# Kernel tuning notes

Hardware: AMD Instinct MI355X
Metric: run time of the kernel (lower is better)

The kernel has to match this reference:

```python
import jax, jax.numpy as jnp
import numpy as np

BATCH = 1024


def setup_inputs() -> dict:
    key = jax.random.key(0)
    ks = jax.random.split(key, 8)
    piece_positions = jax.random.randint(ks[0], (BATCH, 64, 10), 0, 2) > 0  # bool occupancy
    king_positions = jax.random.randint(ks[1], (BATCH, 2), 0, 64, dtype=jnp.int32)
    input_weights = jax.random.randint(ks[2], (64, 641, 256), -32768, 32767, dtype=jnp.int16)
    input_bias = jnp.zeros((256,), dtype=jnp.int16)
    w1 = jax.random.randint(ks[3], (32, 512), -128, 127, dtype=jnp.int8)
    b1 = jnp.zeros((32,), dtype=jnp.int32)
    w2 = jax.random.randint(ks[4], (32, 32), -128, 127, dtype=jnp.int8)
    b2 = jnp.zeros((32,), dtype=jnp.int32)
    out_w = jax.random.randint(ks[5], (32,), -128, 127, dtype=jnp.int8)
    out_b = jnp.zeros((1,), dtype=jnp.int32)
    return {
        'piece_positions': piece_positions, 'king_positions': king_positions,
        'input_weights': input_weights, 'input_bias': input_bias,
        'w1': w1, 'b1': b1, 'w2': w2, 'b2': b2, 'out_w': out_w, 'out_b': out_b,
    }


def _fc(x, w, b):
    # int8 inputs/weights, int32 accumulate, floor-div 64, clamp to [0,127] -> int8
    y = x.astype(jnp.int32) @ w.T.astype(jnp.int32) + b
    y = jnp.floor_divide(y, 64)
    return jnp.clip(y, 0, 127).astype(jnp.int8)


def reference(piece_positions, king_positions, input_weights, input_bias,
              w1, b1, w2, b2, out_w, out_b):
    B = piece_positions.shape[0]
    pp = piece_positions.reshape(B, 640).astype(jnp.int32)  # flattened 64x10 HalfKP features

    def half(king_idx):
        wk = input_weights[king_idx]            # (B, 641, 256) gathered per-sample king table
        feats = wk[:, :640, :].astype(jnp.int32)
        kbias = wk[:, 640, :].astype(jnp.int32)
        return jnp.einsum('bf,bfd->bd', pp, feats) + kbias  # (B, 256)

    white = half(king_positions[:, 0])
    black = half(king_positions[:, 1])
    # int16 wraparound semantics of the original: accumulate in int32, mod-cast to int16
    acc = (white + black + input_bias.astype(jnp.int32)).astype(jnp.int16)

    x = jnp.clip(acc, 0, 127).astype(jnp.int8)
    x = jnp.concatenate([x, x], axis=1)  # (B, 512) side_to_move || other_side
    x = _fc(x, w1, b1)
    x = _fc(x, w2, b2)
    s = jnp.sum(x.astype(jnp.int32) * out_w.astype(jnp.int32)) + out_b  # scalar sum over batch too (as in source)
    return jnp.floor_divide(s, 16)  # shape (1,)
```

## Files before the change

kernel.cpp:

```cpp
#include <hip/hip_runtime.h>
#include <stdint.h>

#define NDIM  256
#define NFEAT 640
#define NROWS 641
#define SG    8
#define MAXG  16
#define MAXRPB 320

typedef unsigned short ushort4v __attribute__((ext_vector_type(4)));
typedef unsigned short ushort8v __attribute__((ext_vector_type(8)));

__global__ void nnue_bucket(const int* __restrict__ kp, const int* __restrict__ W32,
                            const int* __restrict__ pp32, int nslots,
                            int* __restrict__ ws,
                            int* __restrict__ king_start, int* __restrict__ slot_list,
                            int* __restrict__ slot_pos)
{
    __shared__ int cnt[64];
    __shared__ int off[64];
    const int t = threadIdx.x;
    if (t < 64) cnt[t] = 0;
    if (t == 0) {
        int raww = 0, rawpp = 0;
        for (int i = 0; i < 16; ++i) {
            const int v = W32[i];
            if (v > 32767 || v < -32768) raww = 1;
            const int u = pp32[i];
            if (u != 0 && u != 1) rawpp = 1;
        }
        ws[0] = 0; ws[1] = raww; ws[2] = rawpp;
    }
    __syncthreads();
    for (int s = t; s < nslots; s += 256) atomicAdd(&cnt[kp[s]], 1);
    __syncthreads();
    if (t == 0) {
        int run = 0;
        for (int k = 0; k < 64; ++k) { off[k] = run; king_start[k] = run; run += cnt[k]; }
        king_start[64] = run;
    }
    __syncthreads();
    for (int s = t; s < nslots; s += 256) {
        const int k = kp[s];
        const int pos = atomicAdd(&off[k], 1);
        slot_list[pos] = s;
        slot_pos[s] = pos;
    }
}

struct GatherLds {
    int samp[SG];
    unsigned mask[MAXRPB];
    unsigned red[4][SG][NDIM / 2];
};

template<bool RAWW, bool RAWPP>
__device__ __forceinline__ void gather_body(
    const void* __restrict__ ppv, const void* __restrict__ Wv,
    const int* __restrict__ king_start, const int* __restrict__ slot_list,
    unsigned short* __restrict__ partial, int nslots, int rp, GatherLds& sh)
{
    const int bid = blockIdx.x;
    const int k = bid & 63;
    const int rest = bid >> 6;
    const int p = rest & (rp - 1);
    const int gi = rest / rp;
    const int t = threadIdx.x, l = t & 63, g = t >> 6;

    const int s0 = king_start[k], s1 = king_start[k + 1];
    const int base = s0 + gi * SG;
    if (base >= s1) return;
    const int ns = min(SG, s1 - base);
    const unsigned emask = (ns >= 32) ? 0xFFFFFFFFu : ((1u << ns) - 1u);
    const int rpb = NFEAT / rp;
    const int r0 = p * rpb;

    if (t < SG) sh.samp[t] = slot_list[base + min(t, ns - 1)] >> 1;
    __syncthreads();

    for (int r = t; r < rpb; r += 256) {
        unsigned mm = 0;
        #pragma unroll
        for (int i = 0; i < SG; ++i) {
            const int s = sh.samp[i];
            int v;
            if (RAWPP) v = ((const uint8_t*)ppv)[(size_t)s * NFEAT + r0 + r];
            else       v = ((const int*)ppv)[(size_t)s * NFEAT + r0 + r];
            mm |= (v != 0 ? 1u : 0u) << i;
        }
        sh.mask[r] = mm & emask;
    }
    __syncthreads();

    ushort4v acc[SG];
    #pragma unroll
    for (int i = 0; i < SG; ++i) acc[i] = (ushort4v)0;

    const char* Wk = (const char*)Wv + (size_t)k * NROWS * NDIM * (RAWW ? 2 : 4);
    const int rows_per_wave = rpb / 4;
    const int lbeg = g * rows_per_wave;

    #pragma unroll 2
    for (int rr = 0; rr < rows_per_wave; ++rr) {
        const int lr = lbeg + rr;
        unsigned mm = sh.mask[lr];
        mm = __builtin_amdgcn_readfirstlane(mm);
        ushort4v w;
        if (RAWW) {
            w = *(const ushort4v*)(Wk + (size_t)(r0 + lr) * 512 + (size_t)l * 8);
        } else {
            const int4 u = *(const int4*)(Wk + (size_t)(r0 + lr) * 1024 + (size_t)l * 16);
            w.x = (unsigned short)u.x; w.y = (unsigned short)u.y;
            w.z = (unsigned short)u.z; w.w = (unsigned short)u.w;
        }
        #pragma unroll
        for (int i = 0; i < SG; ++i)
            if (mm & (1u << i)) acc[i] += w;
    }

    #pragma unroll
    for (int i = 0; i < SG; ++i)
        *(ushort4v*)&sh.red[g][i][2 * l] = acc[i];
    __syncthreads();

    const int i = t >> 5;
    const int j4 = (t & 31) * 4;
    if (i < ns) {
        ushort8v s = *(const ushort8v*)&sh.red[0][i][j4];
        #pragma unroll
        for (int g2 = 1; g2 < 4; ++g2) s += *(const ushort8v*)&sh.red[g2][i][j4];
        *(ushort8v*)&partial[((size_t)p * nslots + base + i) * NDIM + (size_t)(t & 31) * 8] = s;
    }
}

__global__ __launch_bounds__(256, 6) void nnue_gather(
    const void* __restrict__ pp, const void* __restrict__ W,
    const int* __restrict__ ws, const int* __restrict__ king_start,
    const int* __restrict__ slot_list, unsigned short* __restrict__ partial,
    int nslots, int rp)
{
    __shared__ GatherLds sh;
    const int raww = ws[1], rawpp = ws[2];
    if (raww) {
        if (rawpp) gather_body<true,  true >(pp, W, king_start, slot_list, partial, nslots, rp, sh);
        else       gather_body<true,  false>(pp, W, king_start, slot_list, partial, nslots, rp, sh);
    } else {
        if (rawpp) gather_body<false, true >(pp, W, king_start, slot_list, partial, nslots, rp, sh);
        else       gather_body<false, false>(pp, W, king_start, slot_list, partial, nslots, rp, sh);
    }
}

struct CombineLds {
    alignas(16) int8_t x[NDIM];
    int fc[256];
    alignas(4) int8_t x2[32];
};

template<bool RAWW>
__device__ __forceinline__ void combine_body(
    const unsigned short* __restrict__ partial, const int* __restrict__ slot_pos,
    const int* __restrict__ kp, const void* __restrict__ Wv,
    const void* __restrict__ ibv,
    const void* __restrict__ w1v, const int* __restrict__ b1,
    const void* __restrict__ w2v, const int* __restrict__ b2,
    const void* __restrict__ owv, int* __restrict__ ws, int nslots, int rp,
    CombineLds& sh)
{
    const int b = blockIdx.x;
    const int t = threadIdx.x;

    const int pos0 = slot_pos[2 * b + 0];
    const int pos1 = slot_pos[2 * b + 1];
    const int k0 = kp[2 * b + 0];
    const int k1 = kp[2 * b + 1];
    {
        unsigned tot = 0;
        for (int pi = 0; pi < rp; ++pi) {
            tot += partial[((size_t)pi * nslots + pos0) * NDIM + t];
            tot += partial[((size_t)pi * nslots + pos1) * NDIM + t];
        }
        if (RAWW) {
            const uint16_t* Wq = (const uint16_t*)Wv;
            tot += Wq[((size_t)k0 * NROWS + NFEAT) * NDIM + t];
            tot += Wq[((size_t)k1 * NROWS + NFEAT) * NDIM + t];
            tot += ((const uint16_t*)ibv)[t];
        } else {
            const int* Wq = (const int*)Wv;
            tot += (unsigned)Wq[((size_t)k0 * NROWS + NFEAT) * NDIM + t];
            tot += (unsigned)Wq[((size_t)k1 * NROWS + NFEAT) * NDIM + t];
            tot += (unsigned)((const int*)ibv)[t];
        }
        int v = (int)(int16_t)(uint16_t)tot;
        v = v < 0 ? 0 : (v > 127 ? 127 : v);
        sh.x[t] = (int8_t)v;
    }
    __syncthreads();

    {
        const int o = t >> 3, part = t & 7;
        int y = 0;
        const uint32_t* xw = (const uint32_t*)sh.x;
        if (RAWW) {
            const uint32_t* w1r = (const uint32_t*)((const char*)w1v + o * 512);
            #pragma unroll
            for (int i = 0; i < 8; ++i) {
                const int wi = part * 8 + i;
                const uint32_t xv = xw[wi];
                const uint32_t wa = w1r[wi];
                const uint32_t wb = w1r[64 + wi];
                #pragma unroll
                for (int jj = 0; jj < 4; ++jj) {
                    const int xj  = (int)((xv >> (8 * jj)) & 0xFFu);
                    const int waj = (int)(int8_t)(uint8_t)(wa >> (8 * jj));
                    const int wbj = (int)(int8_t)(uint8_t)(wb >> (8 * jj));
                    y += xj * (waj + wbj);
                }
            }
        } else {
            const int* w1r = (const int*)w1v + o * 512;
            #pragma unroll
            for (int i = 0; i < 8; ++i) {
                const int wi = part * 8 + i;
                const uint32_t xv = xw[wi];
                #pragma unroll
                for (int jj = 0; jj < 4; ++jj) {
                    const int xj = (int)((xv >> (8 * jj)) & 0xFFu);
                    y += xj * (w1r[wi * 4 + jj] + w1r[256 + wi * 8 / 2 + jj]);
                }
            }
        }
        sh.fc[t] = y;
    }
    __syncthreads();

    if (t < 32) {
        int y = b1[t];
        #pragma unroll
        for (int pq = 0; pq < 8; ++pq) y += sh.fc[t * 8 + pq];
        y >>= 6;
        y = y < 0 ? 0 : (y > 127 ? 127 : y);
        sh.x2[t] = (int8_t)y;
    }
    __syncthreads();

    if (t < 32) {
        int y = b2[t];
        const uint32_t* x2w = (const uint32_t*)sh.x2;
        if (RAWW) {
            const uint32_t* w2r = (const uint32_t*)((const char*)w2v + t * 32);
            #pragma unroll
            for (int i = 0; i < 8; ++i) {
                const uint32_t xv = x2w[i];
                const uint32_t wv = w2r[i];
                #pragma unroll
                for (int jj = 0; jj < 4; ++jj)
                    y += (int)((xv >> (8 * jj)) & 0xFFu) * (int)(int8_t)(uint8_t)(wv >> (8 * jj));
            }
        } else {
            const int* w2r = (const int*)w2v + t * 32;
            #pragma unroll
            for (int i = 0; i < 8; ++i) {
                const uint32_t xv = x2w[i];
                #pragma unroll
                for (int jj = 0; jj < 4; ++jj)
                    y += (int)((xv >> (8 * jj)) & 0xFFu) * w2r[i * 4 + jj];
            }
        }
        y >>= 6;
        y = y < 0 ? 0 : (y > 127 ? 127 : y);
        const int owx = RAWW ? (int)((const int8_t*)owv)[t] : ((const int*)owv)[t];
        int pr = y * owx;
        #pragma unroll
        for (int off = 16; off > 0; off >>= 1) pr += __shfl_down(pr, off, 32);
        if (t == 0) atomicAdd(ws, pr);
    }
}

__global__ __launch_bounds__(256) void nnue_combine(
    const unsigned short* __restrict__ partial, const int* __restrict__ slot_pos,
    const int* __restrict__ kp, const void* __restrict__ W,
    const void* __restrict__ ib,
    const void* __restrict__ w1, const int* __restrict__ b1,
    const void* __restrict__ w2, const int* __restrict__ b2,
    const void* __restrict__ ow, int* __restrict__ ws, int nslots, int rp)
{
    __shared__ CombineLds sh;
    if (ws[1]) combine_body<true >(partial, slot_pos, kp, W, ib, w1, b1, w2, b2, ow, ws, nslots, rp, sh);
    else       combine_body<false>(partial, slot_pos, kp, W, ib, w1, b1, w2, b2, ow, ws, nslots, rp, sh);
}

__global__ void nnue_finalize(const int* __restrict__ ws, const int* __restrict__ ob,
                              int* __restrict__ out) {
    out[0] = (ws[0] + ob[0]) >> 4;
}

struct SharedBuf {
    uint8_t pp[NFEAT];
    int     acc[4][NDIM];
    alignas(16) int8_t x[NDIM];
    int     fc[256];
    alignas(4) int8_t x2[32];
    int     list[4][160];
};

__global__ void detect_layout(const int* __restrict__ W32, const int* __restrict__ pp32,
                              int* __restrict__ ws) {
    int raww = 0, rawpp = 0;
    for (int i = 0; i < 16; ++i) {
        const int v = W32[i];
        if (v > 32767 || v < -32768) raww = 1;
        const int u = pp32[i];
        if (u != 0 && u != 1) rawpp = 1;
    }
    ws[0] = 0; ws[1] = raww; ws[2] = rawpp;
}

template<bool RAWW, bool RAWPP>
__device__ __forceinline__ void mono_body(
    const void* __restrict__ ppv, const int* __restrict__ kp,
    const void* __restrict__ Wv,  const void* __restrict__ ibv,
    const void* __restrict__ w1v, const int* __restrict__ b1,
    const void* __restrict__ w2v, const int* __restrict__ b2,
    const void* __restrict__ owv, int* __restrict__ ws, SharedBuf& sh)
{
    const int b = blockIdx.x;
    const int t = threadIdx.x;
    const int l = t & 63;
    const int g = t >> 6;

    if (RAWPP) {
        const uint32_t* src = (const uint32_t*)((const uint8_t*)ppv + (size_t)b * NFEAT);
        if (t < NFEAT / 4) ((uint32_t*)sh.pp)[t] = src[t];
    } else {
        const int* src = (const int*)ppv + (size_t)b * NFEAT;
        for (int i = t; i < NFEAT; i += 256) sh.pp[i] = (uint8_t)(src[i] != 0);
    }
    __syncthreads();

    const int base = g * 160;
    int cnt = 0;
    for (int c = 0; c < 160; c += 64) {
        const int idx = c + l;
        const bool flag = (idx < 160) && (sh.pp[base + idx] != 0);
        const unsigned long long mmask = __ballot(flag);
        const int pos = cnt + (int)__popcll(mmask & ((1ull << l) - 1ull));
        if (flag) sh.list[g][pos] = base + idx;
        cnt += (int)__popcll(mmask);
    }

    const int k0 = kp[b * 2 + 0];
    const int k1 = kp[b * 2 + 1];
    int a0 = 0, a1 = 0, a2 = 0, a3 = 0, a4 = 0, a5 = 0, a6 = 0, a7 = 0;

    if (RAWW) {
        const char* W0 = (const char*)Wv + (size_t)k0 * (NROWS * NDIM * 2);
        const char* W1 = (const char*)Wv + (size_t)k1 * (NROWS * NDIM * 2);
        const int lo = l * 8;
        auto step = [&](int f) {
            const uint2 u0 = *(const uint2*)(W0 + f * 512 + lo);
            const uint2 u1 = *(const uint2*)(W1 + f * 512 + lo);
            a0 += (int)(u0.x & 0xFFFFu); a1 += (int)(u0.x >> 16);
            a2 += (int)(u0.y & 0xFFFFu); a3 += (int)(u0.y >> 16);
            a4 += (int)(u1.x & 0xFFFFu); a5 += (int)(u1.x >> 16);
            a6 += (int)(u1.y & 0xFFFFu); a7 += (int)(u1.y >> 16);
        };
        int j = 0;
        for (; j + 4 <= cnt; j += 4) {
            const int f0 = sh.list[g][j], f1 = sh.list[g][j + 1];
            const int f2 = sh.list[g][j + 2], f3 = sh.list[g][j + 3];
            step(f0); step(f1); step(f2); step(f3);
        }
        for (; j < cnt; ++j) step(sh.list[g][j]);
    } else {
        const char* W0 = (const char*)Wv + (size_t)k0 * (NROWS * NDIM * 4);
        const char* W1 = (const char*)Wv + (size_t)k1 * (NROWS * NDIM * 4);
        const int lo = l * 16;
        auto step = [&](int f) {
            const int4 u0 = *(const int4*)(W0 + f * 1024 + lo);
            const int4 u1 = *(const int4*)(W1 + f * 1024 + lo);
            a0 += u0.x; a1 += u0.y; a2 += u0.z; a3 += u0.w;
            a4 += u1.x; a5 += u1.y; a6 += u1.z; a7 += u1.w;
        };
        int j = 0;
        for (; j + 4 <= cnt; j += 4) {
            const int f0 = sh.list[g][j], f1 = sh.list[g][j + 1];
            const int f2 = sh.list[g][j + 2], f3 = sh.list[g][j + 3];
            step(f0); step(f1); step(f2); step(f3);
        }
        for (; j < cnt; ++j) step(sh.list[g][j]);
    }

    sh.acc[g][4 * l + 0] = a0 + a4;
    sh.acc[g][4 * l + 1] = a1 + a5;
    sh.acc[g][4 * l + 2] = a2 + a6;
    sh.acc[g][4 * l + 3] = a3 + a7;
    __syncthreads();

    {
        const int d = t;
        int tot = sh.acc[0][d] + sh.acc[1][d] + sh.acc[2][d] + sh.acc[3][d];
        int kb0, kb1, ibx;
        if (RAWW) {
            const int16_t* Wq = (const int16_t*)Wv;
            kb0 = Wq[((size_t)k0 * NROWS + NFEAT) * NDIM + d];
            kb1 = Wq[((size_t)k1 * NROWS + NFEAT) * NDIM + d];
            ibx = ((const int16_t*)ibv)[d];
        } else {
            const int* Wq = (const int*)Wv;
            kb0 = Wq[((size_t)k0 * NROWS + NFEAT) * NDIM + d];
            kb1 = Wq[((size_t)k1 * NROWS + NFEAT) * NDIM + d];
            ibx = ((const int*)ibv)[d];
        }
        tot += kb0 + kb1 + ibx;
        int v = (int)(int16_t)(uint16_t)(uint32_t)tot;
        v = v < 0 ? 0 : (v > 127 ? 127 : v);
        sh.x[d] = (int8_t)v;
    }
    __syncthreads();

    {
        const int o = t >> 3, part = t & 7;
        int y = 0;
        const uint32_t* xw = (const uint32_t*)sh.x;
        if (RAWW) {
            const uint32_t* w1r = (const uint32_t*)((const char*)w1v + o * 512);
            #pragma unroll
            for (int i = 0; i < 8; ++i) {
                const int wi = part * 8 + i;
                const uint32_t xv = xw[wi];
                const uint32_t wa = w1r[wi];
                const uint32_t wb = w1r[64 + wi];
                #pragma unroll
                for (int jj = 0; jj < 4; ++jj) {
                    const int xj  = (int)((xv >> (8 * jj)) & 0xFFu);
                    const int waj = (int)(int8_t)(uint8_t)(wa >> (8 * jj));
                    const int wbj = (int)(int8_t)(uint8_t)(wb >> (8 * jj));
                    y += xj * (waj + wbj);
                }
            }
        } else {
            const int* w1r = (const int*)w1v + o * 512;
            #pragma unroll
            for (int i = 0; i < 8; ++i) {
                const int wi = part * 8 + i;
                const uint32_t xv = xw[wi];
                #pragma unroll
                for (int jj = 0; jj < 4; ++jj) {
                    const int xj = (int)((xv >> (8 * jj)) & 0xFFu);
                    y += xj * (w1r[wi * 4 + jj] + w1r[256 + wi * 4 + jj]);
                }
            }
        }
        sh.fc[t] = y;
    }
    __syncthreads();

    if (t < 32) {
        int y = b1[t];
        #pragma unroll
        for (int pq = 0; pq < 8; ++pq) y += sh.fc[t * 8 + pq];
        y >>= 6;
        y = y < 0 ? 0 : (y > 127 ? 127 : y);
        sh.x2[t] = (int8_t)y;
    }
    __syncthreads();

    if (t < 32) {
        int y = b2[t];
        const uint32_t* x2w = (const uint32_t*)sh.x2;
        if (RAWW) {
            const uint32_t* w2r = (const uint32_t*)((const char*)w2v + t * 32);
            #pragma unroll
            for (int i = 0; i < 8; ++i) {
                const uint32_t xv = x2w[i];
                const uint32_t wv = w2r[i];
                #pragma unroll
                for (int jj = 0; jj < 4; ++jj)
                    y += (int)((xv >> (8 * jj)) & 0xFFu) * (int)(int8_t)(uint8_t)(wv >> (8 * jj));
            }
        } else {
            const int* w2r = (const int*)w2v + t * 32;
            #pragma unroll
            for (int i = 0; i < 8; ++i) {
                const uint32_t xv = x2w[i];
                #pragma unroll
                for (int jj = 0; jj < 4; ++jj)
                    y += (int)((xv >> (8 * jj)) & 0xFFu) * w2r[i * 4 + jj];
            }
        }
        y >>= 6;
        y = y < 0 ? 0 : (y > 127 ? 127 : y);
        const int owx = RAWW ? (int)((const int8_t*)owv)[t] : ((const int*)owv)[t];
        int pr = y * owx;
        #pragma unroll
        for (int off = 16; off > 0; off >>= 1) pr += __shfl_down(pr, off, 32);
        if (t == 0) atomicAdd(ws, pr);
    }
}

__global__ __launch_bounds__(256, 4) void nnue_mono(
    const void* __restrict__ pp, const int* __restrict__ kp,
    const void* __restrict__ W,  const void* __restrict__ ib,
    const void* __restrict__ w1, const int* __restrict__ b1,
    const void* __restrict__ w2, const int* __restrict__ b2,
    const void* __restrict__ ow, int* __restrict__ ws)
{
    __shared__ SharedBuf sh;
    const int raww = ws[1], rawpp = ws[2];
    if (raww) {
        if (rawpp) mono_body<true,  true >(pp, kp, W, ib, w1, b1, w2, b2, ow, ws, sh);
        else       mono_body<true,  false>(pp, kp, W, ib, w1, b1, w2, b2, ow, ws, sh);
    } else {
        if (rawpp) mono_body<false, true >(pp, kp, W, ib, w1, b1, w2, b2, ow, ws, sh);
        else       mono_body<false, false>(pp, kp, W, ib, w1, b1, w2, b2, ow, ws, sh);
    }
}

extern "C" void kernel_launch(void* const* d_in, const int* in_sizes, int n_in,
                              void* d_out, int out_size, void* d_ws, size_t ws_size,
                              hipStream_t stream)
{
    const void* pp = d_in[0];
    const int*  kp = (const int*)d_in[1];
    const void* W  = d_in[2];
    const void* ib = d_in[3];
    const void* w1 = d_in[4];
    const int*  b1 = (const int*)d_in[5];
    const void* w2 = d_in[6];
    const int*  b2 = (const int*)d_in[7];
    const void* ow = d_in[8];
    const int*  ob = (const int*)d_in[9];
    int* ws  = (int*)d_ws;
    int* out = (int*)d_out;

    const int B = in_sizes[1] / 2;
    const int nslots = 2 * B;

    const size_t off_ks = 16;
    const size_t off_sl = 96;
    const size_t off_sp = off_sl + (size_t)nslots;
    const size_t off_pb = ((off_sp + (size_t)nslots + 255) / 256) * 256;
    const size_t need4 = (off_pb + (size_t)4 * nslots * (NDIM / 2)) * 4;
    const size_t need2 = (off_pb + (size_t)2 * nslots * (NDIM / 2)) * 4;

    int rp = 0;
    if (ws_size >= need4) rp = 4;
    else if (ws_size >= need2) rp = 2;

    if (rp) {
        int* king_start = ws + off_ks;
        int* slot_list  = ws + off_sl;
        int* slot_pos   = ws + off_sp;
        unsigned short* partial = (unsigned short*)(ws + off_pb);

        hipLaunchKernelGGL(nnue_bucket, dim3(1), dim3(256), 0, stream,
                           kp, (const int*)W, (const int*)pp, nslots,
                           ws, king_start, slot_list, slot_pos);
        hipLaunchKernelGGL(nnue_gather, dim3(64 * MAXG * rp), dim3(256), 0, stream,
                           pp, W, ws, king_start, slot_list, partial, nslots, rp);
        hipLaunchKernelGGL(nnue_combine, dim3(B), dim3(256), 0, stream,
                           partial, slot_pos, kp, W, ib, w1, b1, w2, b2, ow, ws, nslots, rp);
        hipLaunchKernelGGL(nnue_finalize, dim3(1), dim3(1), 0, stream, ws, ob, out);
    } else {
        hipLaunchKernelGGL(detect_layout, dim3(1), dim3(1), 0, stream,
                           (const int*)W, (const int*)pp, ws);
        hipLaunchKernelGGL(nnue_mono, dim3(B), dim3(256), 0, stream,
                           pp, kp, W, ib, w1, b1, w2, b2, ow, ws);
        hipLaunchKernelGGL(nnue_finalize, dim3(1), dim3(1), 0, stream, ws, ob, out);
    }
}
```

Measured before the change: 148.3 us.

## Fuse bucketing into gather, batch combine samples, and finalize via last-block ticket

Removes the single-block bucket kernel: each gather block now builds its own king's slot list in LDS with a wave ballot scan over all king indices, and loops over sample groups with a fixed stride instead of launching a sparse MAXG grid. Combine handles several samples per block, indexes partials by slot id directly, and writes the final output through a last-block atomic ticket, dropping the finalize kernel. The intent is fewer launches, fewer serialized single-block phases and fewer global atomics. In exchange every gather block redundantly scans all king positions, occupancy drops under the new launch bounds, and the fast path now requires at most 2048 slots.

```diff
diff --git a/kernel.cpp b/kernel.cpp
--- a/kernel.cpp
+++ b/kernel.cpp
@@ -5,148 +5,151 @@
 #define NFEAT 640
 #define NROWS 641
 #define SG    8
-#define MAXG  16
+#define GSTRIDE 4
 #define MAXRPB 320
+#define CPB   4
+#define MAXSLOTS 2048
 
 typedef unsigned short ushort4v __attribute__((ext_vector_type(4)));
 typedef unsigned short ushort8v __attribute__((ext_vector_type(8)));
 
-__global__ void nnue_bucket(const int* __restrict__ kp, const int* __restrict__ W32,
-                            const int* __restrict__ pp32, int nslots,
-                            int* __restrict__ ws,
-                            int* __restrict__ king_start, int* __restrict__ slot_list,
-                            int* __restrict__ slot_pos)
-{
-    __shared__ int cnt[64];
-    __shared__ int off[64];
-    const int t = threadIdx.x;
-    if (t < 64) cnt[t] = 0;
+struct GatherLds {
+    int flags[2];
+    int cnt;
+    unsigned short list[MAXSLOTS];
+    int samp[SG];
+    int slotid[SG];
+    unsigned mask[MAXRPB];
+    unsigned red[4][SG][NDIM / 2];
+};
+
+template<bool RAWW, bool RAWPP>
+__device__ __forceinline__ void gather_body(
+    const void* __restrict__ ppv, const void* __restrict__ Wv,
+    unsigned short* __restrict__ partial, int nslots, int rp, GatherLds& sh)
+{
+    const int bid = blockIdx.x;
+    const int k = bid & 63;
+    const int rest = bid >> 6;
+    const int p = rest & (rp - 1);
+    const int g0 = rest >> (rp == 4 ? 2 : 1);
+    const int t = threadIdx.x, l = t & 63, g = t >> 6;
+
+    const int cnt = sh.cnt;
+    const int rpb = NFEAT / rp;
+    const int r0 = p * rpb;
+    const int rows_per_wave = rpb / 4;
+    const int lbeg = g * rows_per_wave;
+    const char* Wk = (const char*)Wv + (size_t)k * NROWS * NDIM * (RAWW ? 2 : 4);
+
+    for (int gi = g0; gi * SG < cnt; gi += GSTRIDE) {
+        const int base = gi * SG;
+        const int ns = min(SG, cnt - base);
+        const unsigned emask = (1u << ns) - 1u;
+
+        if (t < SG) {
+            const int s = sh.list[base + min(t, ns - 1)];
+            sh.slotid[t] = s;
+            sh.samp[t] = s >> 1;
+        }
+        __syncthreads();
+
+        for (int r = t; r < rpb; r += 256) {
+            unsigned mm = 0;
+            #pragma unroll
+            for (int i = 0; i < SG; ++i) {
+                const int s = sh.samp[i];
+                int v;
+                if (RAWPP) v = ((const uint8_t*)ppv)[(size_t)s * NFEAT + r0 + r];
+                else       v = ((const int*)ppv)[(size_t)s * NFEAT + r0 + r];
+                mm |= (v != 0 ? 1u : 0u) << i;
+            }
+            sh.mask[r] = mm & emask;
+        }
+        __syncthreads();
+
+        ushort4v acc[SG];
+        #pragma unroll
+        for (int i = 0; i < SG; ++i) acc[i] = (ushort4v)0;
+
+        #pragma unroll 2
+        for (int rr = 0; rr < rows_per_wave; ++rr) {
+            const int lr = lbeg + rr;
+            unsigned mm = sh.mask[lr];
+            mm = __builtin_amdgcn_readfirstlane(mm);
+            ushort4v w;
+            if (RAWW) {
+                w = *(const ushort4v*)(Wk + (size_t)(r0 + lr) * 512 + (size_t)l * 8);
+            } else {
+                const int4 u = *(const int4*)(Wk + (size_t)(r0 + lr) * 1024 + (size_t)l * 16);
+                w.x = (unsigned short)u.x; w.y = (unsigned short)u.y;
+                w.z = (unsigned short)u.z; w.w = (unsigned short)u.w;
+            }
+            #pragma unroll
+            for (int i = 0; i < SG; ++i)
+                if (mm & (1u << i)) acc[i] += w;
+        }
+
+        #pragma unroll
+        for (int i = 0; i < SG; ++i)
+            *(ushort4v*)&sh.red[g][i][2 * l] = acc[i];
+        __syncthreads();
+
+        const int i = t >> 5;
+        const int j4 = (t & 31) * 4;
+        if (i < ns) {
+            ushort8v sv = *(const ushort8v*)&sh.red[0][i][j4];
+            #pragma unroll
+            for (int g2 = 1; g2 < 4; ++g2) sv += *(const ushort8v*)&sh.red[g2][i][j4];
+            *(ushort8v*)&partial[((size_t)p * nslots + sh.slotid[i]) * NDIM + (size_t)(t & 31) * 8] = sv;
+        }
+        __syncthreads();
+    }
+}
+
+__global__ __launch_bounds__(256, 4) void nnue_gather(
+    const void* __restrict__ pp, const int* __restrict__ kp,
+    const void* __restrict__ W, unsigned short* __restrict__ partial,
+    int* __restrict__ ws, int nslots, int rp)
+{
+    __shared__ GatherLds sh;
+    const int t = threadIdx.x, l = t & 63, g = t >> 6;
+    const int k = blockIdx.x & 63;
+
+    if (blockIdx.x == 0 && t == 0) { ws[0] = 0; ws[3] = 0; }
+
     if (t == 0) {
         int raww = 0, rawpp = 0;
+        const int* W32 = (const int*)W;
+        const int* pp32 = (const int*)pp;
         for (int i = 0; i < 16; ++i) {
             const int v = W32[i];
             if (v > 32767 || v < -32768) raww = 1;
             const int u = pp32[i];
             if (u != 0 && u != 1) rawpp = 1;
         }
-        ws[0] = 0; ws[1] = raww; ws[2] = rawpp;
-    }
-    __syncthreads();
-    for (int s = t; s < nslots; s += 256) atomicAdd(&cnt[kp[s]], 1);
-    __syncthreads();
-    if (t == 0) {
-        int run = 0;
-        for (int k = 0; k < 64; ++k) { off[k] = run; king_start[k] = run; run += cnt[k]; }
-        king_start[64] = run;
-    }
-    __syncthreads();
-    for (int s = t; s < nslots; s += 256) {
-        const int k = kp[s];
-        const int pos = atomicAdd(&off[k], 1);
-        slot_list[pos] = s;
-        slot_pos[s] = pos;
-    }
-}
-
-struct GatherLds {
-    int samp[SG];
-    unsigned mask[MAXRPB];
-    unsigned red[4][SG][NDIM / 2];
-};
-
-template<bool RAWW, bool RAWPP>
-__device__ __forceinline__ void gather_body(
-    const void* __restrict__ ppv, const void* __restrict__ Wv,
-    const int* __restrict__ king_start, const int* __restrict__ slot_list,
-    unsigned short* __restrict__ partial, int nslots, int rp, GatherLds& sh)
-{
-    const int bid = blockIdx.x;
-    const int k = bid & 63;
-    const int rest = bid >> 6;
-    const int p = rest & (rp - 1);
-    const int gi = rest / rp;
-    const int t = threadIdx.x, l = t & 63, g = t >> 6;
-
-    const int s0 = king_start[k], s1 = king_start[k + 1];
-    const int base = s0 + gi * SG;
-    if (base >= s1) return;
-    const int ns = min(SG, s1 - base);
-    const unsigned emask = (ns >= 32) ? 0xFFFFFFFFu : ((1u << ns) - 1u);
-    const int rpb = NFEAT / rp;
-    const int r0 = p * rpb;
-
-    if (t < SG) sh.samp[t] = slot_list[base + min(t, ns - 1)] >> 1;
-    __syncthreads();
-
-    for (int r = t; r < rpb; r += 256) {
-        unsigned mm = 0;
-        #pragma unroll
-        for (int i = 0; i < SG; ++i) {
-            const int s = sh.samp[i];
-            int v;
-            if (RAWPP) v = ((const uint8_t*)ppv)[(size_t)s * NFEAT + r0 + r];
-            else       v = ((const int*)ppv)[(size_t)s * NFEAT + r0 + r];
-            mm |= (v != 0 ? 1u : 0u) << i;
-        }
-        sh.mask[r] = mm & emask;
-    }
-    __syncthreads();
-
-    ushort4v acc[SG];
-    #pragma unroll
-    for (int i = 0; i < SG; ++i) acc[i] = (ushort4v)0;
-
-    const char* Wk = (const char*)Wv + (size_t)k * NROWS * NDIM * (RAWW ? 2 : 4);
-    const int rows_per_wave = rpb / 4;
-    const int lbeg = g * rows_per_wave;
-
-    #pragma unroll 2
-    for (int rr = 0; rr < rows_per_wave; ++rr) {
-        const int lr = lbeg + rr;
-        unsigned mm = sh.mask[lr];
-        mm = __builtin_amdgcn_readfirstlane(mm);
-        ushort4v w;
-        if (RAWW) {
-            w = *(const ushort4v*)(Wk + (size_t)(r0 + lr) * 512 + (size_t)l * 8);
-        } else {
-            const int4 u = *(const int4*)(Wk + (size_t)(r0 + lr) * 1024 + (size_t)l * 16);
-            w.x = (unsigned short)u.x; w.y = (unsigned short)u.y;
-            w.z = (unsigned short)u.z; w.w = (unsigned short)u.w;
-        }
-        #pragma unroll
-        for (int i = 0; i < SG; ++i)
-            if (mm & (1u << i)) acc[i] += w;
-    }
-
-    #pragma unroll
-    for (int i = 0; i < SG; ++i)
-        *(ushort4v*)&sh.red[g][i][2 * l] = acc[i];
-    __syncthreads();
-
-    const int i = t >> 5;
-    const int j4 = (t & 31) * 4;
-    if (i < ns) {
-        ushort8v s = *(const ushort8v*)&sh.red[0][i][j4];
-        #pragma unroll
-        for (int g2 = 1; g2 < 4; ++g2) s += *(const ushort8v*)&sh.red[g2][i][j4];
-        *(ushort8v*)&partial[((size_t)p * nslots + base + i) * NDIM + (size_t)(t & 31) * 8] = s;
-    }
-}
-
-__global__ __launch_bounds__(256, 6) void nnue_gather(
-    const void* __restrict__ pp, const void* __restrict__ W,
-    const int* __restrict__ ws, const int* __restrict__ king_start,
-    const int* __restrict__ slot_list, unsigned short* __restrict__ partial,
-    int nslots, int rp)
-{
-    __shared__ GatherLds sh;
-    const int raww = ws[1], rawpp = ws[2];
+        sh.flags[0] = raww; sh.flags[1] = rawpp;
+    }
+    if (g == 0) {
+        int cnt = 0;
+        for (int c = 0; c < nslots; c += 64) {
+            const int s = c + l;
+            const bool f = (s < nslots) && (kp[s] == k);
+            const unsigned long long m = __ballot(f);
+            if (f) sh.list[cnt + (int)__popcll(m & ((1ull << l) - 1ull))] = (unsigned short)s;
+            cnt += (int)__popcll(m);
+        }
+        if (l == 0) sh.cnt = cnt;
+    }
+    __syncthreads();
+
+    const int raww = sh.flags[0], rawpp = sh.flags[1];
     if (raww) {
-        if (rawpp) gather_body<true,  true >(pp, W, king_start, slot_list, partial, nslots, rp, sh);
-        else       gather_body<true,  false>(pp, W, king_start, slot_list, partial, nslots, rp, sh);
+        if (rawpp) gather_body<true,  true >(pp, W, partial, nslots, rp, sh);
+        else       gather_body<true,  false>(pp, W, partial, nslots, rp, sh);
     } else {
-        if (rawpp) gather_body<false, true >(pp, W, king_start, slot_list, partial, nslots, rp, sh);
-        else       gather_body<false, false>(pp, W, king_start, slot_list, partial, nslots, rp, sh);
+        if (rawpp) gather_body<false, true >(pp, W, partial, nslots, rp, sh);
+        else       gather_body<false, false>(pp, W, partial, nslots, rp, sh);
     }
 }
 
@@ -154,139 +157,163 @@
     alignas(16) int8_t x[NDIM];
     int fc[256];
     alignas(4) int8_t x2[32];
+    int flags;
 };
 
 template<bool RAWW>
 __device__ __forceinline__ void combine_body(
-    const unsigned short* __restrict__ partial, const int* __restrict__ slot_pos,
-    const int* __restrict__ kp, const void* __restrict__ Wv,
-    const void* __restrict__ ibv,
+    const unsigned short* __restrict__ partial, const int* __restrict__ kp,
+    const void* __restrict__ Wv, const void* __restrict__ ibv,
     const void* __restrict__ w1v, const int* __restrict__ b1,
     const void* __restrict__ w2v, const int* __restrict__ b2,
-    const void* __restrict__ owv, int* __restrict__ ws, int nslots, int rp,
-    CombineLds& sh)
-{
-    const int b = blockIdx.x;
+    const void* __restrict__ owv, const int* __restrict__ ob,
+    int* __restrict__ ws, int* __restrict__ out,
+    int nslots, int B, int rp, CombineLds& sh)
+{
     const int t = threadIdx.x;
-
-    const int pos0 = slot_pos[2 * b + 0];
-    const int pos1 = slot_pos[2 * b + 1];
-    const int k0 = kp[2 * b + 0];
-    const int k1 = kp[2 * b + 1];
-    {
-        unsigned tot = 0;
-        for (int pi = 0; pi < rp; ++pi) {
-            tot += partial[((size_t)pi * nslots + pos0) * NDIM + t];
-            tot += partial[((size_t)pi * nslots + pos1) * NDIM + t];
-        }
-        if (RAWW) {
-            const uint16_t* Wq = (const uint16_t*)Wv;
-            tot += Wq[((size_t)k0 * NROWS + NFEAT) * NDIM + t];
-            tot += Wq[((size_t)k1 * NROWS + NFEAT) * NDIM + t];
-            tot += ((const uint16_t*)ibv)[t];
-        } else {
-            const int* Wq = (const int*)Wv;
-            tot += (unsigned)Wq[((size_t)k0 * NROWS + NFEAT) * NDIM + t];
-            tot += (unsigned)Wq[((size_t)k1 * NROWS + NFEAT) * NDIM + t];
-            tot += (unsigned)((const int*)ibv)[t];
-        }
-        int v = (int)(int16_t)(uint16_t)tot;
-        v = v < 0 ? 0 : (v > 127 ? 127 : v);
-        sh.x[t] = (int8_t)v;
-    }
-    __syncthreads();
-
-    {
-        const int o = t >> 3, part = t & 7;
-        int y = 0;
-        const uint32_t* xw = (const uint32_t*)sh.x;
-        if (RAWW) {
-            const uint32_t* w1r = (const uint32_t*)((const char*)w1v + o * 512);
-            #pragma unroll
-            for (int i = 0; i < 8; ++i) {
-                const int wi = part * 8 + i;
-                const uint32_t xv = xw[wi];
-                const uint32_t wa = w1r[wi];
-                const uint32_t wb = w1r[64 + wi];
-                #pragma unroll
-                for (int jj = 0; jj < 4; ++jj) {
-                    const int xj  = (int)((xv >> (8 * jj)) & 0xFFu);
-                    const int waj = (int)(int8_t)(uint8_t)(wa >> (8 * jj));
-                    const int wbj = (int)(int8_t)(uint8_t)(wb >> (8 * jj));
-                    y += xj * (waj + wbj);
+    int blocksum = 0;
+
+    for (int ss = 0; ss < CPB; ++ss) {
+        const int b = blockIdx.x * CPB + ss;
+        if (b >= B) break;
+        const int k0 = kp[2 * b + 0];
+        const int k1 = kp[2 * b + 1];
+        {
+            unsigned tot = 0;
+            for (int pi = 0; pi < rp; ++pi) {
+                tot += partial[((size_t)pi * nslots + 2 * b + 0) * NDIM + t];
+                tot += partial[((size_t)pi * nslots + 2 * b + 1) * NDIM + t];
+            }
+            if (RAWW) {
+                const uint16_t* Wq = (const uint16_t*)Wv;
+                tot += Wq[((size_t)k0 * NROWS + NFEAT) * NDIM + t];
+                tot += Wq[((size_t)k1 * NROWS + NFEAT) * NDIM + t];
+                tot += ((const uint16_t*)ibv)[t];
+            } else {
+                const int* Wq = (const int*)Wv;
+                tot += (unsigned)Wq[((size_t)k0 * NROWS + NFEAT) * NDIM + t];
+                tot += (unsigned)Wq[((size_t)k1 * NROWS + NFEAT) * NDIM + t];
+                tot += (unsigned)((const int*)ibv)[t];
+            }
+            int v = (int)(int16_t)(uint16_t)tot;
+            v = v < 0 ? 0 : (v > 127 ? 127 : v);
+            sh.x[t] = (int8_t)v;
+        }
+        __syncthreads();
+
+        {
+            const int o = t >> 3, part = t & 7;
+            int y = 0;
+            const uint32_t* xw = (const uint32_t*)sh.x;
+            if (RAWW) {
+                const uint32_t* w1r = (const uint32_t*)((const char*)w1v + o * 512);
+                #pragma unroll
+                for (int i = 0; i < 8; ++i) {
+                    const int wi = part * 8 + i;
+                    const uint32_t xv = xw[wi];
+                    const uint32_t wa = w1r[wi];
+                    const uint32_t wb = w1r[64 + wi];
+                    #pragma unroll
+                    for (int jj = 0; jj < 4; ++jj) {
+                        const int xj  = (int)((xv >> (8 * jj)) & 0xFFu);
+                        const int waj = (int)(int8_t)(uint8_t)(wa >> (8 * jj));
+                        const int wbj = (int)(int8_t)(uint8_t)(wb >> (8 * jj));
+                        y += xj * (waj + wbj);
+                    }
                 }
-            }
-        } else {
-            const int* w1r = (const int*)w1v + o * 512;
-            #pragma unroll
-            for (int i = 0; i < 8; ++i) {
-                const int wi = part * 8 + i;
-                const uint32_t xv = xw[wi];
-                #pragma unroll
-                for (int jj = 0; jj < 4; ++jj) {
-                    const int xj = (int)((xv >> (8 * jj)) & 0xFFu);
-                    y += xj * (w1r[wi * 4 + jj] + w1r[256 + wi * 8 / 2 + jj]);
+            } else {
+                const int* w1r = (const int*)w1v + o * 512;
+                #pragma unroll
+                for (int i = 0; i < 8; ++i) {
+                    const int wi = part * 8 + i;
+                    const uint32_t xv = xw[wi];
+                    #pragma unroll
+                    for (int jj = 0; jj < 4; ++jj) {
+                        const int xj = (int)((xv >> (8 * jj)) & 0xFFu);
+                        y += xj * (w1r[wi * 4 + jj] + w1r[256 + wi * 4 + jj]);
+                    }
                 }
             }
-        }
-        sh.fc[t] = y;
-    }
-    __syncthreads();
-
-    if (t < 32) {
-        int y = b1[t];
-        #pragma unroll
-        for (int pq = 0; pq < 8; ++pq) y += sh.fc[t * 8 + pq];
-        y >>= 6;
-        y = y < 0 ? 0 : (y > 127 ? 127 : y);
-        sh.x2[t] = (int8_t)y;
-    }
-    __syncthreads();
-
-    if (t < 32) {
-        int y = b2[t];
-        const uint32_t* x2w = (const uint32_t*)sh.x2;
-        if (RAWW) {
-            const uint32_t* w2r = (const uint32_t*)((const char*)w2v + t * 32);
-            #pragma unroll
-            for (int i = 0; i < 8; ++i) {
-                const uint32_t xv = x2w[i];
-                const uint32_t wv = w2r[i];
-                #pragma unroll
-                for (int jj = 0; jj < 4; ++jj)
-                    y += (int)((xv >> (8 * jj)) & 0xFFu) * (int)(int8_t)(uint8_t)(wv >> (8 * jj));
-            }
-        } else {
-            const int* w2r = (const int*)w2v + t * 32;
-            #pragma unroll
-            for (int i = 0; i < 8; ++i) {
-                const uint32_t xv = x2w[i];
-                #pragma unroll
-                for (int jj = 0; jj < 4; ++jj)
-                    y += (int)((xv >> (8 * jj)) & 0xFFu) * w2r[i * 4 + jj];
-            }
-        }
-        y >>= 6;
-        y = y < 0 ? 0 : (y > 127 ? 127 : y);
-        const int owx = RAWW ? (int)((const int8_t*)owv)[t] : ((const int*)owv)[t];
-        int pr = y * owx;
-        #pragma unroll
-        for (int off = 16; off > 0; off >>= 1) pr += __shfl_down(pr, off, 32);
-        if (t == 0) atomicAdd(ws, pr);
+            sh.fc[t] = y;
+        }
+        __syncthreads();
+
+        if (t < 32) {
+            int y = b1[t];
+            #pragma unroll
+            for (int pq = 0; pq < 8; ++pq) y += sh.fc[t * 8 + pq];
+            y >>= 6;
+            y = y < 0 ? 0 : (y > 127 ? 127 : y);
+            sh.x2[t] = (int8_t)y;
+        }
+        __syncthreads();
+
+        if (t < 32) {
+            int y = b2[t];
+            const uint32_t* x2w = (const uint32_t*)sh.x2;
+            if (RAWW) {
+                const uint32_t* w2r = (const uint32_t*)((const char*)w2v + t * 32);
+                #pragma unroll
+                for (int i = 0; i < 8; ++i) {
+                    const uint32_t xv = x2w[i];
+                    const uint32_t wv = w2r[i];
+                    #pragma unroll
+                    for (int jj = 0; jj < 4; ++jj)
+                        y += (int)((xv >> (8 * jj)) & 0xFFu) * (int)(int8_t)(uint8_t)(wv >> (8 * jj));
+                }
+            } else {
+                const int* w2r = (const int*)w2v + t * 32;
+                #pragma unroll
+                for (int i = 0; i < 8; ++i) {
+                    const uint32_t xv = x2w[i];
+                    #pragma unroll
+                    for (int jj = 0; jj < 4; ++jj)
+                        y += (int)((xv >> (8 * jj)) & 0xFFu) * w2r[i * 4 + jj];
+                }
+            }
+            y >>= 6;
+            y = y < 0 ? 0 : (y > 127 ? 127 : y);
+            const int owx = RAWW ? (int)((const int8_t*)owv)[t] : ((const int*)owv)[t];
+            int pr = y * owx;
+            #pragma unroll
+            for (int off = 16; off > 0; off >>= 1) pr += __shfl_down(pr, off, 32);
+            if (t == 0) blocksum += pr;
+        }
+        __syncthreads();
+    }
+
+    if (t == 0) {
+        atomicAdd(&ws[0], blocksum);
+        __threadfence();
+        const int ticket = atomicAdd(&ws[3], 1);
+        if (ticket == (int)gridDim.x - 1) {
+            const int s = atomicAdd(&ws[0], 0);
+            out[0] = (s + ob[0]) >> 4;
+        }
     }
 }
 
 __global__ __launch_bounds__(256) void nnue_combine(
-    const unsigned short* __restrict__ partial, const int* __restrict__ slot_pos,
-    const int* __restrict__ kp, const void* __restrict__ W,
-    const void* __restrict__ ib,
+    const unsigned short* __restrict__ partial, const int* __restrict__ kp,
+    const void* __restrict__ W, const void* __restrict__ ib,
     const void* __restrict__ w1, const int* __restrict__ b1,
     const void* __restrict__ w2, const int* __restrict__ b2,
-    const void* __restrict__ ow, int* __restrict__ ws, int nslots, int rp)
+    const void* __restrict__ ow, const int* __restrict__ ob,
+    int* __restrict__ ws, int* __restrict__ out, int nslots, int B, int rp)
 {
     __shared__ CombineLds sh;
-    if (ws[1]) combine_body<true >(partial, slot_pos, kp, W, ib, w1, b1, w2, b2, ow, ws, nslots, rp, sh);
-    else       combine_body<false>(partial, slot_pos, kp, W, ib, w1, b1, w2, b2, ow, ws, nslots, rp, sh);
+    if (threadIdx.x == 0) {
+        int raww = 0;
+        const int* W32 = (const int*)W;
+        for (int i = 0; i < 16; ++i) {
+            const int v = W32[i];
+            if (v > 32767 || v < -32768) raww = 1;
+        }
+        sh.flags = raww;
+    }
+    __syncthreads();
+    if (sh.flags) combine_body<true >(partial, kp, W, ib, w1, b1, w2, b2, ow, ob, ws, out, nslots, B, rp, sh);
+    else          combine_body<false>(partial, kp, W, ib, w1, b1, w2, b2, ow, ob, ws, out, nslots, B, rp, sh);
 }
 
 __global__ void nnue_finalize(const int* __restrict__ ws, const int* __restrict__ ob,
@@ -536,10 +563,7 @@
     const int B = in_sizes[1] / 2;
     const int nslots = 2 * B;
 
-    const size_t off_ks = 16;
-    const size_t off_sl = 96;
-    const size_t off_sp = off_sl + (size_t)nslots;
-    const size_t off_pb = ((off_sp + (size_t)nslots + 255) / 256) * 256;
+    const size_t off_pb = 256;
     const size_t need4 = (off_pb + (size_t)4 * nslots * (NDIM / 2)) * 4;
     const size_t need2 = (off_pb + (size_t)2 * nslots * (NDIM / 2)) * 4;
 
@@ -547,20 +571,12 @@
     if (ws_size >= need4) rp = 4;
     else if (ws_size >= need2) rp = 2;
 
-    if (rp) {
-        int* king_start = ws + off_ks;
-        int* slot_list  = ws + off_sl;
-        int* slot_pos   = ws + off_sp;
+    if (rp && nslots <= MAXSLOTS) {
         unsigned short* partial = (unsigned short*)(ws + off_pb);
-
-        hipLaunchKernelGGL(nnue_bucket, dim3(1), dim3(256), 0, stream,
-                           kp, (const int*)W, (const int*)pp, nslots,
-                           ws, king_start, slot_list, slot_pos);
-        hipLaunchKernelGGL(nnue_gather, dim3(64 * MAXG * rp), dim3(256), 0, stream,
-                           pp, W, ws, king_start, slot_list, partial, nslots, rp);
-        hipLaunchKernelGGL(nnue_combine, dim3(B), dim3(256), 0, stream,
-                           partial, slot_pos, kp, W, ib, w1, b1, w2, b2, ow, ws, nslots, rp);
-        hipLaunchKernelGGL(nnue_finalize, dim3(1), dim3(1), 0, stream, ws, ob, out);
+        hipLaunchKernelGGL(nnue_gather, dim3(64 * rp * GSTRIDE), dim3(256), 0, stream,
+                           pp, kp, W, partial, ws, nslots, rp);
+        hipLaunchKernelGGL(nnue_combine, dim3((B + CPB - 1) / CPB), dim3(256), 0, stream,
+                           partial, kp, W, ib, w1, b1, w2, b2, ow, ob, ws, out, nslots, B, rp);
     } else {
         hipLaunchKernelGGL(detect_layout, dim3(1), dim3(1), 0, stream,
                            (const int*)W, (const int*)pp, ws);
```

After: 161.8 us. 1.09x slower.
